# Optimization experiments

Hardware: AMD Instinct MI355X
Metric: run time of the kernel (lower is better)

## Reference

```python
import jax, jax.numpy as jnp
import numpy as np

N = 8192
IN_F = 512
OUT_F = 256
ALPHA = 0.2          # LeakyReLU negative slope
MASK_VAL = -9e15     # same sentinel as the torch code


def setup_inputs() -> dict:
    key = jax.random.key(0)
    k1, k2, k3, k4, k5, k6 = jax.random.split(key, 6)
    inputs = jax.random.normal(k1, (N, IN_F), dtype=jnp.float32)
    # sparse-ish 0/1 dense adjacency (~avg degree 64)
    adj = (jax.random.uniform(k2, (N, N)) < (64.0 / N)).astype(jnp.float32)
    W = jax.random.normal(k3, (IN_F, OUT_F), dtype=jnp.float32) * (1.414 / np.sqrt(IN_F))
    a = jax.random.normal(k4, (2 * OUT_F, 1), dtype=jnp.float32) * 0.1
    W_gc = jax.random.normal(k5, (IN_F, OUT_F), dtype=jnp.float32) * (1.414 / np.sqrt(IN_F))
    b_gc = jax.random.normal(k6, (OUT_F,), dtype=jnp.float32) * 0.01
    return {"inputs": inputs, "adj": adj, "W": W, "a": a, "W_gc": W_gc, "b_gc": b_gc}


def reference(inputs, adj, W, a, W_gc, b_gc):
    # h: [n, F]
    h = inputs @ W
    F = h.shape[1]
    # Fused additive attention: e[i,j] = leaky_relu(a1.h_i + a2.h_j)
    # (mathematically identical to the repeat/cat construction in the source)
    f_src = h @ a[:F, 0]   # [n]
    f_dst = h @ a[F:, 0]   # [n]
    e = jax.nn.leaky_relu(f_src[:, None] + f_dst[None, :], negative_slope=ALPHA)  # [n, n]
    # masked row-softmax over neighbors
    att = jnp.where(adj > 0, e, MASK_VAL)
    att = jax.nn.softmax(att, axis=1)
    # dropout p=0.0 -> identity
    h_prime = att @ h  # [n, F]
    # optional dense graph-convolution branch (graph_convolve=True)
    gc = adj @ (inputs @ W_gc) + b_gc
    return h_prime + gc
```

## Files before the change

kernel.cpp:

```cpp
#include <hip/hip_runtime.h>
#include <hip/hip_bf16.h>
#include <math.h>

#define N_NODES 8192
#define IN_F    512
#define OUT_F   256
#define NCAT    512
#define ALPHA   0.2f
#define MAXDEG  512

typedef __attribute__((ext_vector_type(8))) short short8;
typedef __attribute__((ext_vector_type(4))) float f32x4;

static __device__ __forceinline__ short f2bf(float f) {
    union { float f; unsigned u; } v; v.f = f;
    unsigned r = v.u + 0x7fffu + ((v.u >> 16) & 1u);
    return (short)(r >> 16);
}
static __device__ __forceinline__ float bf2f(short s) {
    union { unsigned u; float f; } v;
    v.u = ((unsigned)(unsigned short)s) << 16;
    return v.f;
}

__global__ __launch_bounds__(512) void bt_pack(const float* __restrict__ W,
                                               const float* __restrict__ W_gc,
                                               short* __restrict__ Bt) {
    const int n = blockIdx.x;
    const int k = threadIdx.x;
    const int c = n >> 1;
    float v = (n & 1) ? W_gc[(size_t)k * OUT_F + c] : W[(size_t)k * OUT_F + c];
    Bt[(size_t)n * IN_F + k] = f2bf(v);
}

__global__ __launch_bounds__(256) void gemm_mfma(const float* __restrict__ A,
                                                 const short* __restrict__ Bt,
                                                 short* __restrict__ hcat) {
    __shared__ short As[128 * 32];
    __shared__ short Bs[128 * 32];

    const int tid  = threadIdx.x;
    const int m0   = blockIdx.y * 128;
    const int n0   = blockIdx.x * 128;
    const int wid  = tid >> 6;
    const int lane = tid & 63;
    const int wr   = wid >> 1;
    const int wc   = wid & 1;
    const int mh   = lane & 15;
    const int q    = lane >> 4;

    const int srow  = tid >> 1;
    const int shalf = tid & 1;

    const f32x4 vzero = {0.f, 0.f, 0.f, 0.f};
    f32x4 acc[4][4];
    #pragma unroll
    for (int i = 0; i < 4; i++)
        #pragma unroll
        for (int j = 0; j < 4; j++) acc[i][j] = vzero;

    const float* aga = A  + (size_t)(m0 + srow) * IN_F + shalf * 16;
    const short* bgb = Bt + (size_t)(n0 + srow) * IN_F + shalf * 16;
    short* asw = &As[srow * 32 + shalf * 16];
    short* bsw = &Bs[srow * 32 + shalf * 16];

    for (int k0 = 0; k0 < IN_F; k0 += 32) {
        const float4* a4 = (const float4*)(aga + k0);
        float4 x0 = a4[0], x1 = a4[1], x2 = a4[2], x3 = a4[3];
        const int4* b4 = (const int4*)(bgb + k0);
        int4 bv0 = b4[0], bv1 = b4[1];

        short8 p0, p1;
        p0[0] = f2bf(x0.x); p0[1] = f2bf(x0.y); p0[2] = f2bf(x0.z); p0[3] = f2bf(x0.w);
        p0[4] = f2bf(x1.x); p0[5] = f2bf(x1.y); p0[6] = f2bf(x1.z); p0[7] = f2bf(x1.w);
        p1[0] = f2bf(x2.x); p1[1] = f2bf(x2.y); p1[2] = f2bf(x2.z); p1[3] = f2bf(x2.w);
        p1[4] = f2bf(x3.x); p1[5] = f2bf(x3.y); p1[6] = f2bf(x3.z); p1[7] = f2bf(x3.w);

        __syncthreads();
        *(short8*)asw       = p0;
        *(short8*)(asw + 8) = p1;
        *(int4*)bsw         = bv0;
        *(int4*)(bsw + 8)   = bv1;
        __syncthreads();

        short8 af[4], bfm[4];
        #pragma unroll
        for (int i = 0; i < 4; i++) {
            af[i]  = *(const short8*)&As[(wr * 64 + i * 16 + mh) * 32 + q * 8];
            bfm[i] = *(const short8*)&Bs[(wc * 64 + i * 16 + mh) * 32 + q * 8];
        }
        #pragma unroll
        for (int mi = 0; mi < 4; mi++)
            #pragma unroll
            for (int ni = 0; ni < 4; ni++)
                acc[mi][ni] = __builtin_amdgcn_mfma_f32_16x16x32_bf16(
                    af[mi], bfm[ni], acc[mi][ni], 0, 0, 0);
    }

    #pragma unroll
    for (int mi = 0; mi < 4; mi++)
        #pragma unroll
        for (int ni = 0; ni < 4; ni++) {
            const int col   = n0 + wc * 64 + ni * 16 + mh;
            const int rbase = m0 + wr * 64 + mi * 16 + q * 4;
            f32x4 v = acc[mi][ni];
            #pragma unroll
            for (int r = 0; r < 4; r++)
                hcat[(size_t)(rbase + r) * NCAT + col] = f2bf(v[r]);
        }
}

__global__ __launch_bounds__(256) void compute_f(const short* __restrict__ hcat,
                                                 const float* __restrict__ a,
                                                 float* __restrict__ f_src,
                                                 float* __restrict__ f_dst) {
    const int row  = blockIdx.x * 4 + (threadIdx.x >> 6);
    const int lane = threadIdx.x & 63;
    const short* hr = hcat + (size_t)row * NCAT;
    float s1 = 0.f, s2 = 0.f;
    #pragma unroll
    for (int c = lane; c < OUT_F; c += 64) {
        float hv = bf2f(hr[2 * c]);
        s1 += hv * a[c];
        s2 += hv * a[OUT_F + c];
    }
    #pragma unroll
    for (int off = 32; off; off >>= 1) {
        s1 += __shfl_down(s1, off);
        s2 += __shfl_down(s2, off);
    }
    if (lane == 0) { f_src[row] = s1; f_dst[row] = s2; }
}

__global__ __launch_bounds__(256) void attn_row(const float* __restrict__ adj,
                                                const short* __restrict__ hcat,
                                                const float* __restrict__ f_src,
                                                const float* __restrict__ f_dst,
                                                const float* __restrict__ b_gc,
                                                float* __restrict__ out) {
    __shared__ int   s_idx[MAXDEG];
    __shared__ float s_w[MAXDEG];
    __shared__ float s_red[8];
    __shared__ int   s_count;
    __shared__ float s_part[4][64][9];

    const int row  = blockIdx.x;
    const int tid  = threadIdx.x;
    const int lane = tid & 63;
    const int wid  = tid >> 6;

    if (tid == 0) s_count = 0;
    __syncthreads();

    const float4* arow4 = (const float4*)(adj + (size_t)row * N_NODES);
    for (int c = tid; c < N_NODES / 4; c += 256) {
        float4 v = arow4[c];
        int cnt = (v.x > 0.f) + (v.y > 0.f) + (v.z > 0.f) + (v.w > 0.f);
        if (cnt) {
            int pos = atomicAdd(&s_count, cnt);
            const int j0 = c * 4;
            if (v.x > 0.f && pos < MAXDEG) s_idx[pos++] = j0;
            if (v.y > 0.f && pos < MAXDEG) s_idx[pos++] = j0 + 1;
            if (v.z > 0.f && pos < MAXDEG) s_idx[pos++] = j0 + 2;
            if (v.w > 0.f && pos < MAXDEG) s_idx[pos++] = j0 + 3;
        }
    }
    __syncthreads();
    const int deg = min(s_count, MAXDEG);

    const float fs = f_src[row];
    float lmax = -INFINITY;
    for (int k = tid; k < deg; k += 256) {
        const int j = s_idx[k];
        float e = fs + f_dst[j];
        e = (e > 0.f) ? e : ALPHA * e;
        s_w[k] = e;
        lmax = fmaxf(lmax, e);
    }
    #pragma unroll
    for (int off = 32; off; off >>= 1) lmax = fmaxf(lmax, __shfl_down(lmax, off));
    if (lane == 0) s_red[wid] = lmax;
    __syncthreads();
    const float m = fmaxf(fmaxf(s_red[0], s_red[1]), fmaxf(s_red[2], s_red[3]));

    float lsum = 0.f;
    for (int k = tid; k < deg; k += 256) {
        float w = __expf(s_w[k] - m);
        s_w[k] = w;
        lsum += w;
    }
    #pragma unroll
    for (int off = 32; off; off >>= 1) lsum += __shfl_down(lsum, off);
    if (lane == 0) s_red[4 + wid] = lsum;
    __syncthreads();
    const float l = s_red[4] + s_red[5] + s_red[6] + s_red[7];
    const float inv_l = (deg > 0) ? 1.f / l : 0.f;

    const int p = lane;
    float aa[4] = {0.f, 0.f, 0.f, 0.f};
    float gg[4] = {0.f, 0.f, 0.f, 0.f};
    for (int k = wid; k < deg; k += 4) {
        const int   j = s_idx[k];
        const float w = s_w[k];
        short8 v = *(const short8*)(hcat + (size_t)j * NCAT + p * 8);
        aa[0] += w * bf2f(v[0]); gg[0] += bf2f(v[1]);
        aa[1] += w * bf2f(v[2]); gg[1] += bf2f(v[3]);
        aa[2] += w * bf2f(v[4]); gg[2] += bf2f(v[5]);
        aa[3] += w * bf2f(v[6]); gg[3] += bf2f(v[7]);
    }
    #pragma unroll
    for (int i = 0; i < 4; i++) {
        s_part[wid][p][i]     = aa[i];
        s_part[wid][p][4 + i] = gg[i];
    }
    __syncthreads();

    const int c  = tid;
    const int pg = c >> 2, ci = c & 3;
    float a_tot = s_part[0][pg][ci]     + s_part[1][pg][ci]
                + s_part[2][pg][ci]     + s_part[3][pg][ci];
    float g_tot = s_part[0][pg][4 + ci] + s_part[1][pg][4 + ci]
                + s_part[2][pg][4 + ci] + s_part[3][pg][4 + ci];
    out[(size_t)row * OUT_F + c] = a_tot * inv_l + g_tot + b_gc[c];
}

extern "C" void kernel_launch(void* const* d_in, const int* in_sizes, int n_in,
                              void* d_out, int out_size, void* d_ws, size_t ws_size,
                              hipStream_t stream) {
    const float* inputs = (const float*)d_in[0];
    const float* adj    = (const float*)d_in[1];
    const float* W      = (const float*)d_in[2];
    const float* a      = (const float*)d_in[3];
    const float* W_gc   = (const float*)d_in[4];
    const float* b_gc   = (const float*)d_in[5];
    float* out = (float*)d_out;

    short* Bt    = (short*)d_ws;
    short* hcat  = Bt + (size_t)NCAT * IN_F;
    float* f_src = (float*)(hcat + (size_t)N_NODES * NCAT);
    float* f_dst = f_src + N_NODES;

    bt_pack<<<dim3(NCAT), dim3(IN_F), 0, stream>>>(W, W_gc, Bt);
    gemm_mfma<<<dim3(NCAT / 128, N_NODES / 128), 256, 0, stream>>>(inputs, Bt, hcat);
    compute_f<<<N_NODES / 4, 256, 0, stream>>>(hcat, a, f_src, f_dst);
    attn_row<<<N_NODES, 256, 0, stream>>>(adj, hcat, f_src, f_dst, b_gc, out);
}
```

Before: 430.7 us.

## Fuse neighbor scan with logit compute and split gather across waves by column

The adjacency row scan is now fully unrolled with nontemporal loads, and it computes the LeakyReLU logits and the running max inline. This removes one block barrier and a second pass over the neighbor list. The gather stage is repartitioned: each wave owns a 128-element slice of the concatenated row, and its four 16-lane groups stride over neighbors and reduce with shuffles. This replaces the shared-memory partial buffer and the final barrier, and the output is written with float4 stores. The trade-off is that each neighbor's row read is now split into 16-lane 256-byte pieces across waves rather than one 1 KB read per wave, which may change memory coalescing.

```diff
diff --git a/kernel.cpp b/kernel.cpp
--- a/kernel.cpp
+++ b/kernel.cpp
@@ -142,7 +142,6 @@
     __shared__ float s_w[MAXDEG];
     __shared__ float s_red[8];
     __shared__ int   s_count;
-    __shared__ float s_part[4][64][9];
 
     const int row  = blockIdx.x;
     const int tid  = threadIdx.x;
@@ -152,36 +151,37 @@
     if (tid == 0) s_count = 0;
     __syncthreads();
 
-    const float4* arow4 = (const float4*)(adj + (size_t)row * N_NODES);
-    for (int c = tid; c < N_NODES / 4; c += 256) {
-        float4 v = arow4[c];
-        int cnt = (v.x > 0.f) + (v.y > 0.f) + (v.z > 0.f) + (v.w > 0.f);
+    const float fs = f_src[row];
+
+    const f32x4* arow4 = (const f32x4*)(adj + (size_t)row * N_NODES);
+    float lmax = -INFINITY;
+    #pragma unroll
+    for (int it = 0; it < N_NODES / 4 / 256; it++) {
+        const int c = it * 256 + tid;
+        f32x4 v = __builtin_nontemporal_load(arow4 + c);
+        int cnt = (v[0] > 0.f) + (v[1] > 0.f) + (v[2] > 0.f) + (v[3] > 0.f);
         if (cnt) {
             int pos = atomicAdd(&s_count, cnt);
             const int j0 = c * 4;
-            if (v.x > 0.f && pos < MAXDEG) s_idx[pos++] = j0;
-            if (v.y > 0.f && pos < MAXDEG) s_idx[pos++] = j0 + 1;
-            if (v.z > 0.f && pos < MAXDEG) s_idx[pos++] = j0 + 2;
-            if (v.w > 0.f && pos < MAXDEG) s_idx[pos++] = j0 + 3;
+            #pragma unroll
+            for (int i = 0; i < 4; i++) {
+                if (v[i] > 0.f) {
+                    float e = fs + f_dst[j0 + i];
+                    e = (e > 0.f) ? e : ALPHA * e;
+                    s_idx[pos] = j0 + i;
+                    s_w[pos]   = e;
+                    pos++;
+                    lmax = fmaxf(lmax, e);
+                }
+            }
         }
-    }
-    __syncthreads();
-    const int deg = min(s_count, MAXDEG);
-
-    const float fs = f_src[row];
-    float lmax = -INFINITY;
-    for (int k = tid; k < deg; k += 256) {
-        const int j = s_idx[k];
-        float e = fs + f_dst[j];
-        e = (e > 0.f) ? e : ALPHA * e;
-        s_w[k] = e;
-        lmax = fmaxf(lmax, e);
     }
     #pragma unroll
     for (int off = 32; off; off >>= 1) lmax = fmaxf(lmax, __shfl_down(lmax, off));
     if (lane == 0) s_red[wid] = lmax;
     __syncthreads();
-    const float m = fmaxf(fmaxf(s_red[0], s_red[1]), fmaxf(s_red[2], s_red[3]));
+    const float m   = fmaxf(fmaxf(s_red[0], s_red[1]), fmaxf(s_red[2], s_red[3]));
+    const int   deg = min(s_count, MAXDEG);
 
     float lsum = 0.f;
     for (int k = tid; k < deg; k += 256) {
@@ -196,32 +196,41 @@
     const float l = s_red[4] + s_red[5] + s_red[6] + s_red[7];
     const float inv_l = (deg > 0) ? 1.f / l : 0.f;
 
-    const int p = lane;
-    float aa[4] = {0.f, 0.f, 0.f, 0.f};
-    float gg[4] = {0.f, 0.f, 0.f, 0.f};
-    for (int k = wid; k < deg; k += 4) {
+    const int u = lane >> 4;
+    const int p = lane & 15;
+    const short* hbase = hcat + wid * 128 + p * 8;
+
+    float aa0 = 0.f, aa1 = 0.f, aa2 = 0.f, aa3 = 0.f;
+    float gg0 = 0.f, gg1 = 0.f, gg2 = 0.f, gg3 = 0.f;
+    #pragma unroll 4
+    for (int k = u; k < deg; k += 4) {
         const int   j = s_idx[k];
         const float w = s_w[k];
-        short8 v = *(const short8*)(hcat + (size_t)j * NCAT + p * 8);
-        aa[0] += w * bf2f(v[0]); gg[0] += bf2f(v[1]);
-        aa[1] += w * bf2f(v[2]); gg[1] += bf2f(v[3]);
-        aa[2] += w * bf2f(v[4]); gg[2] += bf2f(v[5]);
-        aa[3] += w * bf2f(v[6]); gg[3] += bf2f(v[7]);
-    }
-    #pragma unroll
-    for (int i = 0; i < 4; i++) {
-        s_part[wid][p][i]     = aa[i];
-        s_part[wid][p][4 + i] = gg[i];
-    }
-    __syncthreads();
-
-    const int c  = tid;
-    const int pg = c >> 2, ci = c & 3;
-    float a_tot = s_part[0][pg][ci]     + s_part[1][pg][ci]
-                + s_part[2][pg][ci]     + s_part[3][pg][ci];
-    float g_tot = s_part[0][pg][4 + ci] + s_part[1][pg][4 + ci]
-                + s_part[2][pg][4 + ci] + s_part[3][pg][4 + ci];
-    out[(size_t)row * OUT_F + c] = a_tot * inv_l + g_tot + b_gc[c];
+        short8 v = *(const short8*)(hbase + (size_t)j * NCAT);
+        aa0 += w * bf2f(v[0]); gg0 += bf2f(v[1]);
+        aa1 += w * bf2f(v[2]); gg1 += bf2f(v[3]);
+        aa2 += w * bf2f(v[4]); gg2 += bf2f(v[5]);
+        aa3 += w * bf2f(v[6]); gg3 += bf2f(v[7]);
+    }
+    aa0 += __shfl_down(aa0, 32); aa1 += __shfl_down(aa1, 32);
+    aa2 += __shfl_down(aa2, 32); aa3 += __shfl_down(aa3, 32);
+    gg0 += __shfl_down(gg0, 32); gg1 += __shfl_down(gg1, 32);
+    gg2 += __shfl_down(gg2, 32); gg3 += __shfl_down(gg3, 32);
+    aa0 += __shfl_down(aa0, 16); aa1 += __shfl_down(aa1, 16);
+    aa2 += __shfl_down(aa2, 16); aa3 += __shfl_down(aa3, 16);
+    gg0 += __shfl_down(gg0, 16); gg1 += __shfl_down(gg1, 16);
+    gg2 += __shfl_down(gg2, 16); gg3 += __shfl_down(gg3, 16);
+
+    if (u == 0) {
+        const int col = wid * 64 + p * 4;
+        const float4 bg = *(const float4*)(b_gc + col);
+        float4 o;
+        o.x = aa0 * inv_l + gg0 + bg.x;
+        o.y = aa1 * inv_l + gg1 + bg.y;
+        o.z = aa2 * inv_l + gg2 + bg.z;
+        o.w = aa3 * inv_l + gg3 + bg.w;
+        *(float4*)(out + (size_t)row * OUT_F + col) = o;
+    }
 }
 
 extern "C" void kernel_launch(void* const* d_in, const int* in_sizes, int n_in,
```

Result: no change. 432.5 us (+0.4%).
